# Optimization experiments

Measured on AMD Instinct MI355X. Metric: run time of the kernel, lower is better.

Reference implementation:

```python
import jax, jax.numpy as jnp
import numpy as np

N_NODES = 50000
N_EDGES = 800000
IN_DIM = 128
HID = 256
HEADS = 4
OUT_DIM = 128
NEG_SLOPE = 0.2


def gat_conv(x, src, dst, W, a_src, a_dst, b, heads, out_ch):
    """PyG-style GATConv: per-edge attention + segment softmax over dst."""
    N = x.shape[0]
    h = (x @ W).reshape(N, heads, out_ch)              # [N,H,C]
    alph_s = jnp.einsum('nhc,hc->nh', h, a_src)        # [N,H]
    alph_d = jnp.einsum('nhc,hc->nh', h, a_dst)        # [N,H]
    e = jax.nn.leaky_relu(alph_s[src] + alph_d[dst], NEG_SLOPE)  # [E,H]
    m = jax.lax.stop_gradient(jax.ops.segment_max(e, dst, num_segments=N))
    ex = jnp.exp(e - m[dst])
    s = jax.ops.segment_sum(ex, dst, num_segments=N)
    alpha = ex / (s[dst] + 1e-16)                      # [E,H]
    out = jax.ops.segment_sum(h[src] * alpha[:, :, None], dst, num_segments=N)
    return out.reshape(N, heads * out_ch) + b


def setup_inputs() -> dict:
    key = jax.random.key(0)
    ks = jax.random.split(key, 12)
    x = jax.random.normal(ks[0], (N_NODES, IN_DIM), dtype=jnp.float32)
    edge_index = jax.random.randint(ks[1], (2, N_EDGES), 0, N_NODES, dtype=jnp.int64)
    c1 = HID // HEADS  # 64
    sc1 = 1.0 / np.sqrt(IN_DIM)
    sc2 = 1.0 / np.sqrt(HID)
    W1 = jax.random.normal(ks[2], (IN_DIM, HID), dtype=jnp.float32) * sc1
    a1_src = jax.random.normal(ks[3], (HEADS, c1), dtype=jnp.float32) * sc1
    a1_dst = jax.random.normal(ks[4], (HEADS, c1), dtype=jnp.float32) * sc1
    b1 = jnp.zeros((HID,), dtype=jnp.float32)
    W2 = jax.random.normal(ks[5], (HID, OUT_DIM), dtype=jnp.float32) * sc2
    a2_src = jax.random.normal(ks[6], (1, OUT_DIM), dtype=jnp.float32) * sc2
    a2_dst = jax.random.normal(ks[7], (1, OUT_DIM), dtype=jnp.float32) * sc2
    b2 = jnp.zeros((OUT_DIM,), dtype=jnp.float32)
    return {"x": x, "edge_index": edge_index, "W1": W1, "a1_src": a1_src,
            "a1_dst": a1_dst, "b1": b1, "W2": W2, "a2_src": a2_src,
            "a2_dst": a2_dst, "b2": b2}


def reference(x, edge_index, W1, a1_src, a1_dst, b1, W2, a2_src, a2_dst, b2):
    N = x.shape[0]
    loops = jnp.arange(N, dtype=edge_index.dtype)
    # PyG default add_self_loops=True
    src = jnp.concatenate([edge_index[0], loops])
    dst = jnp.concatenate([edge_index[1], loops])
    h = jax.nn.relu(gat_conv(x, src, dst, W1, a1_src, a1_dst, b1, HEADS, HID // HEADS))
    # dropout is identity in eval mode
    return gat_conv(h, src, dst, W2, a2_src, a2_dst, b2, 1, OUT_DIM)
```

## Files before the change

### kernel.cpp

```cpp
#include <hip/hip_runtime.h>
#include <math.h>

#define NEG_SLOPE 0.2f
#define SLOTS 64

typedef __attribute__((ext_vector_type(8))) short bf16x8;
typedef __attribute__((ext_vector_type(4))) float f32x4;
typedef __attribute__((ext_vector_type(2))) float f32x2;

__device__ __forceinline__ float lrelu(float t) {
    return t > 0.f ? t : NEG_SLOPE * t;
}
__device__ __forceinline__ float bf2f(unsigned short u) {
    return __uint_as_float(((unsigned)u) << 16);
}
__device__ __forceinline__ unsigned short f2bf(float f) {
    unsigned u = __float_as_uint(f);
    unsigned r = (u + 0x7fff + ((u >> 16) & 1)) >> 16;
    return (unsigned short)r;
}
__device__ __forceinline__ int rli(int v, int l) {
    return __builtin_amdgcn_readlane(v, l);
}
__device__ __forceinline__ f32x2 unpack2(unsigned v) {
    f32x2 r;
    r.x = __uint_as_float(v << 16);
    r.y = __uint_as_float(v & 0xffff0000u);
    return r;
}

__global__ void prep(const float* __restrict__ x, unsigned* __restrict__ x_bf2,
                     const float* __restrict__ W1, unsigned short* __restrict__ W1t,
                     const float* __restrict__ W2, unsigned short* __restrict__ W2t,
                     const float* __restrict__ a1s, const float* __restrict__ a1d,
                     float* __restrict__ vsd1,
                     const float* __restrict__ a2s, const float* __restrict__ a2d,
                     float* __restrict__ vsd2,
                     int* __restrict__ cursor, int* __restrict__ eSrc,
                     long nx2, int N, int n0, int n1, int n2, int n3, int n4) {
    const int b = blockIdx.x, t = threadIdx.x;
    if (b < n0) {
        long i = (long)b * 256 + t;
        if (i < nx2) {
            float2 v = ((const float2*)x)[i];
            x_bf2[i] = (unsigned)f2bf(v.x) | ((unsigned)f2bf(v.y) << 16);
        }
    } else if (b < n1) {
        int i = (b - n0) * 256 + t;
        if (i < 256 * 128) {
            int n = i / 128, k = i % 128;
            W1t[i] = f2bf(W1[k * 256 + n]);
        }
    } else if (b < n2) {
        int i = (b - n1) * 256 + t;
        if (i < 128 * 256) {
            int n = i / 256, k = i % 256;
            W2t[i] = f2bf(W2[k * 128 + n]);
        }
    } else if (b < n3) {
        int i = (b - n2) * 256 + t;
        if (i < 512) {
            int k = i / 4, h = i % 4;
            float s = 0.f, d = 0.f;
            for (int c = 0; c < 64; c++) {
                float wv = W1[k * 256 + h * 64 + c];
                s += wv * a1s[h * 64 + c];
                d += wv * a1d[h * 64 + c];
            }
            vsd1[h * 128 + k] = s;
            vsd1[(4 + h) * 128 + k] = d;
        }
    } else if (b < n4) {
        int i = (b - n3) * 256 + t;
        if (i < 256) {
            float s = 0.f, d = 0.f;
            for (int c = 0; c < 128; c++) {
                float wv = W2[i * 128 + c];
                s += wv * a2s[c];
                d += wv * a2d[c];
            }
            vsd2[i] = s;
            vsd2[256 + i] = d;
        }
    } else {
        int i = (b - n4) * 256 + t;
        if (i < N) {
            cursor[i] = 1;
            eSrc[i << 6] = i;
        }
    }
}

__global__ void scatter_edges(const int* __restrict__ src, const int* __restrict__ dst,
                              int* __restrict__ cursor, int* __restrict__ eSrc, int E) {
    int e = blockIdx.x * blockDim.x + threadIdx.x;
    if (e < E) {
        int d = dst[e];
        int pos = atomicAdd(&cursor[d], 1);
        if (pos < SLOTS) eSrc[(d << 6) + pos] = src[e];
    }
}

template <int K, int H>
__global__ void gemv_attn(const float* __restrict__ X, const float* __restrict__ vsd,
                          float* __restrict__ as_, float* __restrict__ ad_, int M) {
    __shared__ float vs[2 * H * K];
    int t = threadIdx.x;
    for (int i = t; i < 2 * H * K; i += 256) vs[i] = vsd[i];
    __syncthreads();
    int wave = t >> 6, lane = t & 63;
    int n = blockIdx.x * 4 + wave;
    if (n >= M) return;
    float acc[2 * H];
#pragma unroll
    for (int j = 0; j < 2 * H; j++) acc[j] = 0.f;
#pragma unroll
    for (int i = 0; i < K / 64; i++) {
        float xv = X[(size_t)n * K + i * 64 + lane];
#pragma unroll
        for (int j = 0; j < 2 * H; j++) acc[j] += xv * vs[j * K + i * 64 + lane];
    }
#pragma unroll
    for (int off = 32; off > 0; off >>= 1) {
#pragma unroll
        for (int j = 0; j < 2 * H; j++) acc[j] += __shfl_down(acc[j], off, 64);
    }
    if (lane == 0) {
#pragma unroll
        for (int h = 0; h < H; h++) {
            as_[n * H + h] = acc[h];
            ad_[n * H + h] = acc[H + h];
        }
    }
}

template <int K, int N>
__global__ __launch_bounds__(256) void gemm_mfma(const unsigned short* __restrict__ A,
                                                 const unsigned short* __restrict__ Bt,
                                                 unsigned short* __restrict__ Cb, int M) {
    constexpr int LDT = 72;
    __shared__ __align__(16) short As[128 * LDT];
    __shared__ __align__(16) short Bs[64 * LDT];
    const int t = threadIdx.x;
    const int wave = t >> 6, lane = t & 63;
    const int row0 = blockIdx.x * 128;
    const int n0 = blockIdx.y * 64;

    f32x4 acc[2][4];
#pragma unroll
    for (int mt = 0; mt < 2; mt++)
#pragma unroll
        for (int nt = 0; nt < 4; nt++) acc[mt][nt] = (f32x4){0.f, 0.f, 0.f, 0.f};

    const int r = t >> 3, c8 = (t & 7) * 8;
    for (int kc = 0; kc < K; kc += 64) {
        const unsigned short* srcA = A + (size_t)row0 * K + kc;
#pragma unroll
        for (int p = 0; p < 4; p++) {
            int rr = r + p * 32;
            *(bf16x8*)&As[rr * LDT + c8] = *(const bf16x8*)&srcA[(size_t)rr * K + c8];
        }
        const unsigned short* srcB = Bt + (size_t)n0 * K + kc;
#pragma unroll
        for (int p = 0; p < 2; p++) {
            int rr = r + p * 32;
            *(bf16x8*)&Bs[rr * LDT + c8] = *(const bf16x8*)&srcB[(size_t)rr * K + c8];
        }
        __syncthreads();

        const int mbase = wave * 32 + (lane & 15);
        const int quad = lane >> 4;
#pragma unroll
        for (int ks = 0; ks < 2; ks++) {
            int ko = ks * 32 + quad * 8;
            bf16x8 a0 = *(const bf16x8*)&As[mbase * LDT + ko];
            bf16x8 a1 = *(const bf16x8*)&As[(mbase + 16) * LDT + ko];
#pragma unroll
            for (int nt = 0; nt < 4; nt++) {
                bf16x8 b = *(const bf16x8*)&Bs[((lane & 15) + nt * 16) * LDT + ko];
                acc[0][nt] = __builtin_amdgcn_mfma_f32_16x16x32_bf16(a0, b, acc[0][nt], 0, 0, 0);
                acc[1][nt] = __builtin_amdgcn_mfma_f32_16x16x32_bf16(a1, b, acc[1][nt], 0, 0, 0);
            }
        }
        __syncthreads();
    }

    const int colb = n0 + (lane & 15);
    const int rquad = (lane >> 4) * 4;
#pragma unroll
    for (int mt = 0; mt < 2; mt++) {
        int rb = row0 + wave * 32 + mt * 16 + rquad;
#pragma unroll
        for (int nt = 0; nt < 4; nt++) {
#pragma unroll
            for (int rr2 = 0; rr2 < 4; rr2++) {
                int row = rb + rr2;
                if (row < M) Cb[(size_t)row * N + colb + nt * 16] = f2bf(acc[mt][nt][rr2]);
            }
        }
    }
}

__global__ __launch_bounds__(256) void gemm1_head(
    const unsigned short* __restrict__ agg, const unsigned short* __restrict__ W1t,
    const float* __restrict__ b1, const float* __restrict__ vsd2,
    unsigned short* __restrict__ out1b, float* __restrict__ as2, float* __restrict__ ad2,
    int M, int Mpad) {
    constexpr int K = 128, LDT = 72;
    __shared__ __align__(16) short As[128 * LDT];
    __shared__ __align__(16) short Bs[64 * LDT];
    const int t = threadIdx.x;
    const int wave = t >> 6, lane = t & 63;
    const int row0 = blockIdx.x * 128;
    const int h = blockIdx.y;
    const unsigned short* A = agg + (size_t)h * Mpad * K;
    const unsigned short* Bt = W1t + (size_t)h * 64 * K;

    f32x4 acc[2][4];
#pragma unroll
    for (int mt = 0; mt < 2; mt++)
#pragma unroll
        for (int nt = 0; nt < 4; nt++) acc[mt][nt] = (f32x4){0.f, 0.f, 0.f, 0.f};

    const int r = t >> 3, c8 = (t & 7) * 8;
    for (int kc = 0; kc < K; kc += 64) {
        const unsigned short* srcA = A + (size_t)row0 * K + kc;
#pragma unroll
        for (int p = 0; p < 4; p++) {
            int rr = r + p * 32;
            *(bf16x8*)&As[rr * LDT + c8] = *(const bf16x8*)&srcA[(size_t)rr * K + c8];
        }
        const unsigned short* srcB = Bt + kc;
#pragma unroll
        for (int p = 0; p < 2; p++) {
            int rr = r + p * 32;
            *(bf16x8*)&Bs[rr * LDT + c8] = *(const bf16x8*)&srcB[(size_t)rr * K + c8];
        }
        __syncthreads();

        const int mbase = wave * 32 + (lane & 15);
        const int quad = lane >> 4;
#pragma unroll
        for (int ks = 0; ks < 2; ks++) {
            int ko = ks * 32 + quad * 8;
            bf16x8 a0 = *(const bf16x8*)&As[mbase * LDT + ko];
            bf16x8 a1 = *(const bf16x8*)&As[(mbase + 16) * LDT + ko];
#pragma unroll
            for (int nt = 0; nt < 4; nt++) {
                bf16x8 b = *(const bf16x8*)&Bs[((lane & 15) + nt * 16) * LDT + ko];
                acc[0][nt] = __builtin_amdgcn_mfma_f32_16x16x32_bf16(a0, b, acc[0][nt], 0, 0, 0);
                acc[1][nt] = __builtin_amdgcn_mfma_f32_16x16x32_bf16(a1, b, acc[1][nt], 0, 0, 0);
            }
        }
        __syncthreads();
    }

    const int col16 = lane & 15;
    const int grp = lane >> 4;
#pragma unroll
    for (int mt = 0; mt < 2; mt++) {
        int rb = row0 + wave * 32 + mt * 16 + grp * 4;
#pragma unroll
        for (int rr = 0; rr < 4; rr++) {
            int row = rb + rr;
            float ps = 0.f, pd = 0.f;
#pragma unroll
            for (int nt = 0; nt < 4; nt++) {
                int cg = h * 64 + col16 + nt * 16;
                float rres = acc[mt][nt][rr] + b1[cg];
                rres = fmaxf(rres, 0.f);
                if (row < M) out1b[(size_t)row * 256 + cg] = f2bf(rres);
                ps += rres * vsd2[cg];
                pd += rres * vsd2[256 + cg];
            }
#pragma unroll
            for (int mask = 1; mask < 16; mask <<= 1) {
                ps += __shfl_xor(ps, mask, 64);
                pd += __shfl_xor(pd, mask, 64);
            }
            if (col16 == 0 && row < M) {
                atomicAdd(&as2[row], ps);
                atomicAdd(&ad2[row], pd);
            }
        }
    }
}

__global__ __launch_bounds__(256) void fused_gather1(
    const int* __restrict__ cursor, const int* __restrict__ eSrc,
    const unsigned short* __restrict__ Xb,
    const float* __restrict__ as_, const float* __restrict__ ad_,
    unsigned short* __restrict__ agg, int N, int Mpad) {
    const int wv = threadIdx.x >> 6, lane = threadIdx.x & 63;
    const int d = blockIdx.x * 4 + wv;
    if (d >= N) return;
    const int beg = d << 6;
    int deg = cursor[d]; deg = deg > SLOTS ? SLOTS : deg;

    __shared__ float4 alS[4][64];

    float4 adv = ((const float4*)ad_)[d];
    const char* Xc = (const char*)Xb;
    const int loff = lane * 4;

    f32x2 acc[4];
#pragma unroll
    for (int h = 0; h < 4; h++) acc[h] = (f32x2){0.f, 0.f};

    bool act = lane < deg;
    int s = act ? eSrc[beg + lane] : 0;
    int esb = s << 8;
    float4 q = act ? ((const float4*)as_)[s] : make_float4(0.f, 0.f, 0.f, 0.f);
    float e0 = act ? lrelu(q.x + adv.x) : -1e30f;
    float e1 = act ? lrelu(q.y + adv.y) : -1e30f;
    float e2 = act ? lrelu(q.z + adv.z) : -1e30f;
    float e3 = act ? lrelu(q.w + adv.w) : -1e30f;
    float m0 = e0, m1 = e1, m2 = e2, m3 = e3;
#pragma unroll
    for (int off = 1; off < 64; off <<= 1) {
        m0 = fmaxf(m0, __shfl_xor(m0, off, 64));
        m1 = fmaxf(m1, __shfl_xor(m1, off, 64));
        m2 = fmaxf(m2, __shfl_xor(m2, off, 64));
        m3 = fmaxf(m3, __shfl_xor(m3, off, 64));
    }
    float x0 = act ? __expf(e0 - m0) : 0.f;
    float x1 = act ? __expf(e1 - m1) : 0.f;
    float x2 = act ? __expf(e2 - m2) : 0.f;
    float x3 = act ? __expf(e3 - m3) : 0.f;
    float s0 = x0, s1 = x1, s2 = x2, s3 = x3;
#pragma unroll
    for (int off = 1; off < 64; off <<= 1) {
        s0 += __shfl_xor(s0, off, 64);
        s1 += __shfl_xor(s1, off, 64);
        s2 += __shfl_xor(s2, off, 64);
        s3 += __shfl_xor(s3, off, 64);
    }
    if (act) {
        float4 av;
        av.x = x0 / (s0 + 1e-16f);
        av.y = x1 / (s1 + 1e-16f);
        av.z = x2 / (s2 + 1e-16f);
        av.w = x3 / (s3 + 1e-16f);
        alS[wv][lane] = av;
    }

    int j = 0;
    for (; j + 3 < deg; j += 4) {
        int o0 = rli(esb, j), o1 = rli(esb, j + 1);
        int o2 = rli(esb, j + 2), o3 = rli(esb, j + 3);
        unsigned v0 = *(const unsigned*)(Xc + o0 + loff);
        unsigned v1 = *(const unsigned*)(Xc + o1 + loff);
        unsigned v2 = *(const unsigned*)(Xc + o2 + loff);
        unsigned v3 = *(const unsigned*)(Xc + o3 + loff);
        float4 al0 = alS[wv][j];
        float4 al1 = alS[wv][j + 1];
        float4 al2 = alS[wv][j + 2];
        float4 al3 = alS[wv][j + 3];
        f32x2 xv0 = unpack2(v0);
        acc[0] += al0.x * xv0; acc[1] += al0.y * xv0;
        acc[2] += al0.z * xv0; acc[3] += al0.w * xv0;
        f32x2 xv1 = unpack2(v1);
        acc[0] += al1.x * xv1; acc[1] += al1.y * xv1;
        acc[2] += al1.z * xv1; acc[3] += al1.w * xv1;
        f32x2 xv2 = unpack2(v2);
        acc[0] += al2.x * xv2; acc[1] += al2.y * xv2;
        acc[2] += al2.z * xv2; acc[3] += al2.w * xv2;
        f32x2 xv3 = unpack2(v3);
        acc[0] += al3.x * xv3; acc[1] += al3.y * xv3;
        acc[2] += al3.z * xv3; acc[3] += al3.w * xv3;
    }
    for (; j < deg; j++) {
        int o0 = rli(esb, j);
        unsigned v0 = *(const unsigned*)(Xc + o0 + loff);
        float4 al0 = alS[wv][j];
        f32x2 xv0 = unpack2(v0);
        acc[0] += al0.x * xv0; acc[1] += al0.y * xv0;
        acc[2] += al0.z * xv0; acc[3] += al0.w * xv0;
    }

#pragma unroll
    for (int h = 0; h < 4; h++) {
        unsigned pack = (unsigned)f2bf(acc[h].x) | ((unsigned)f2bf(acc[h].y) << 16);
        unsigned* p = (unsigned*)(agg + ((size_t)h * Mpad + d) * 128);
        p[lane] = pack;
    }
}

__global__ __launch_bounds__(256) void fused_gather2(
    const int* __restrict__ cursor, const int* __restrict__ eSrc,
    const unsigned short* __restrict__ Hb,
    const float* __restrict__ as_, const float* __restrict__ ad_,
    const float* __restrict__ b2, float* __restrict__ out, int N) {
    const int wv = threadIdx.x >> 6, lane = threadIdx.x & 63;
    const int d = blockIdx.x * 4 + wv;
    if (d >= N) return;
    const int beg = d << 6;
    int deg = cursor[d]; deg = deg > SLOTS ? SLOTS : deg;

    __shared__ float alS[4][64];

    const float adv = ad_[d];
    const char* Hc = (const char*)Hb;
    const int loff = lane * 4;
    f32x2 acc = (f32x2){0.f, 0.f};

    bool act = lane < deg;
    int s = act ? eSrc[beg + lane] : 0;
    int esb = s << 8;
    float e0 = act ? lrelu(as_[s] + adv) : -1e30f;
    float m0 = e0;
#pragma unroll
    for (int off = 1; off < 64; off <<= 1) m0 = fmaxf(m0, __shfl_xor(m0, off, 64));
    float x0 = act ? __expf(e0 - m0) : 0.f;
    float s0 = x0;
#pragma unroll
    for (int off = 1; off < 64; off <<= 1) s0 += __shfl_xor(s0, off, 64);
    if (act) alS[wv][lane] = x0 / (s0 + 1e-16f);

    int j = 0;
    for (; j + 3 < deg; j += 4) {
        int o0 = rli(esb, j), o1 = rli(esb, j + 1);
        int o2 = rli(esb, j + 2), o3 = rli(esb, j + 3);
        unsigned v0 = *(const unsigned*)(Hc + o0 + loff);
        unsigned v1 = *(const unsigned*)(Hc + o1 + loff);
        unsigned v2 = *(const unsigned*)(Hc + o2 + loff);
        unsigned v3 = *(const unsigned*)(Hc + o3 + loff);
        float b0 = alS[wv][j], b1 = alS[wv][j + 1];
        float b2v = alS[wv][j + 2], b3 = alS[wv][j + 3];
        acc += b0 * unpack2(v0);
        acc += b1 * unpack2(v1);
        acc += b2v * unpack2(v2);
        acc += b3 * unpack2(v3);
    }
    for (; j < deg; j++) {
        int o0 = rli(esb, j);
        unsigned v0 = *(const unsigned*)(Hc + o0 + loff);
        acc += alS[wv][j] * unpack2(v0);
    }

    float2 o;
    o.x = acc.x + b2[lane * 2];
    o.y = acc.y + b2[lane * 2 + 1];
    ((float2*)(out + (size_t)d * 128))[lane] = o;
}

extern "C" void kernel_launch(void* const* d_in, const int* in_sizes, int n_in,
                              void* d_out, int out_size, void* d_ws, size_t ws_size,
                              hipStream_t stream) {
    const float* x   = (const float*)d_in[0];
    const int*   ei  = (const int*)d_in[1];
    const float* W1  = (const float*)d_in[2];
    const float* a1s = (const float*)d_in[3];
    const float* a1d = (const float*)d_in[4];
    const float* b1  = (const float*)d_in[5];
    const float* W2  = (const float*)d_in[6];
    const float* a2s = (const float*)d_in[7];
    const float* a2d = (const float*)d_in[8];
    const float* b2  = (const float*)d_in[9];

    const int N = in_sizes[0] / 128;
    const int E = in_sizes[1] / 2;
    const int* srcIdx = ei;
    const int* dstIdx = ei + E;
    float* out = (float*)d_out;

    const int MT = (N + 127) / 128;
    const int M_pad = MT * 128;

    char* w = (char*)d_ws;
    unsigned short* x_bf  = (unsigned short*)w; w += (size_t)N * 128 * 2;
    unsigned short* agg   = (unsigned short*)w; w += (size_t)4 * M_pad * 128 * 2;
    unsigned short* out1b = (unsigned short*)w; w += (size_t)M_pad * 256 * 2;
    unsigned short* h2b   = (unsigned short*)w; w += (size_t)N * 128 * 2;
    unsigned short* W1t   = (unsigned short*)w; w += (size_t)128 * 256 * 2;
    unsigned short* W2t   = (unsigned short*)w; w += (size_t)256 * 128 * 2;
    float* vsd1 = (float*)w; w += (size_t)128 * 8 * 4;
    float* vsd2 = (float*)w; w += (size_t)256 * 2 * 4;
    float* as1  = (float*)w; w += (size_t)N * 4 * 4;
    float* ad1  = (float*)w; w += (size_t)N * 4 * 4;
    float* as2  = (float*)w; w += (size_t)N * 4;
    float* ad2  = (float*)w; w += (size_t)N * 4;
    int* cursor = (int*)w;  w += (size_t)N * 4;
    int* eSrc   = (int*)w;  w += (size_t)N * SLOTS * 4;

    hipMemsetAsync(as2, 0, (size_t)N * 4, stream);
    hipMemsetAsync(ad2, 0, (size_t)N * 4, stream);

    {
        long nx2 = (long)N * 64;
        int c0 = (int)((nx2 + 255) / 256);
        int n0 = c0;
        int n1 = n0 + 128;
        int n2 = n1 + 128;
        int n3 = n2 + 2;
        int n4 = n3 + 1;
        int total = n4 + (N + 255) / 256;
        prep<<<total, 256, 0, stream>>>(x, (unsigned*)x_bf, W1, W1t, W2, W2t,
                                        a1s, a1d, vsd1, a2s, a2d, vsd2,
                                        cursor, eSrc, nx2, N, n0, n1, n2, n3, n4);
    }

    scatter_edges<<<(E + 255) / 256, 256, 0, stream>>>(srcIdx, dstIdx, cursor, eSrc, E);

    gemv_attn<128, 4><<<(N + 3) / 4, 256, 0, stream>>>(x, vsd1, as1, ad1, N);
    fused_gather1<<<(N + 3) / 4, 256, 0, stream>>>(cursor, eSrc, x_bf, as1, ad1, agg, N, M_pad);
    gemm1_head<<<dim3(MT, 4), 256, 0, stream>>>(agg, W1t, b1, vsd2, out1b, as2, ad2, N, M_pad);

    gemm_mfma<256, 128><<<dim3(MT, 2), 256, 0, stream>>>(out1b, W2t, h2b, N);
    fused_gather2<<<(N + 3) / 4, 256, 0, stream>>>(cursor, eSrc, h2b, as2, ad2, b2, out, N);
}
```

Measured before the change: 301.4 us.

## Process two destination nodes per wavefront with 8-byte gathers in GAT aggregation

Both gather kernels now assign one destination node to each 32-lane half of a wavefront instead of a full 64-lane wave. Each lane loads 8 bytes (4 bf16) per neighbor row, and source offsets are staged in LDS instead of read with readlane. The aim is to double useful lanes per wave for average degree around 17, where most of the 64 lanes sat idle, and to widen the memory transactions. In exchange, each half loops to the larger degree of the pair, adding some wasted iterations and extra LDS traffic.

```diff
diff --git a/kernel.cpp b/kernel.cpp
--- a/kernel.cpp
+++ b/kernel.cpp
@@ -10,17 +10,11 @@
 
 __device__ __forceinline__ float lrelu(float t) {
     return t > 0.f ? t : NEG_SLOPE * t;
-}
-__device__ __forceinline__ float bf2f(unsigned short u) {
-    return __uint_as_float(((unsigned)u) << 16);
 }
 __device__ __forceinline__ unsigned short f2bf(float f) {
     unsigned u = __float_as_uint(f);
     unsigned r = (u + 0x7fff + ((u >> 16) & 1)) >> 16;
     return (unsigned short)r;
-}
-__device__ __forceinline__ int rli(int v, int l) {
-    return __builtin_amdgcn_readlane(v, l);
 }
 __device__ __forceinline__ f32x2 unpack2(unsigned v) {
     f32x2 r;
@@ -292,97 +286,131 @@
     const float* __restrict__ as_, const float* __restrict__ ad_,
     unsigned short* __restrict__ agg, int N, int Mpad) {
     const int wv = threadIdx.x >> 6, lane = threadIdx.x & 63;
-    const int d = blockIdx.x * 4 + wv;
-    if (d >= N) return;
+    const int half = lane >> 5, hl = lane & 31;
+    const int d = blockIdx.x * 8 + wv * 2 + half;
+
+    __shared__ float4 alS[4][2][64];
+    __shared__ int offS[4][2][64];
+
+    const bool vn = d < N;
+    int deg = 0;
+    if (vn) { deg = cursor[d]; if (deg > SLOTS) deg = SLOTS; }
+    float4 adv = make_float4(0.f, 0.f, 0.f, 0.f);
+    if (vn) adv = ((const float4*)ad_)[d];
+
     const int beg = d << 6;
-    int deg = cursor[d]; deg = deg > SLOTS ? SLOTS : deg;
-
-    __shared__ float4 alS[4][64];
-
-    float4 adv = ((const float4*)ad_)[d];
+    const int j0 = hl, j1 = hl + 32;
+    const bool a0 = j0 < deg, a1 = j1 < deg;
+    int s0 = vn ? d : 0, s1 = vn ? d : 0;
+    if (a0) s0 = eSrc[beg + j0];
+    if (a1) s1 = eSrc[beg + j1];
+    float4 q0 = make_float4(0.f, 0.f, 0.f, 0.f), q1 = q0;
+    if (a0) q0 = ((const float4*)as_)[s0];
+    if (a1) q1 = ((const float4*)as_)[s1];
+
+    float qa0[4] = {q0.x, q0.y, q0.z, q0.w};
+    float qa1[4] = {q1.x, q1.y, q1.z, q1.w};
+    float ad4[4] = {adv.x, adv.y, adv.z, adv.w};
+    float e0[4], e1[4], m[4];
+#pragma unroll
+    for (int h = 0; h < 4; h++) {
+        e0[h] = a0 ? lrelu(qa0[h] + ad4[h]) : -1e30f;
+        e1[h] = a1 ? lrelu(qa1[h] + ad4[h]) : -1e30f;
+        m[h] = fmaxf(e0[h], e1[h]);
+    }
+#pragma unroll
+    for (int off = 1; off < 32; off <<= 1)
+#pragma unroll
+        for (int h = 0; h < 4; h++) m[h] = fmaxf(m[h], __shfl_xor(m[h], off, 64));
+    float x0[4], x1[4], sum[4];
+#pragma unroll
+    for (int h = 0; h < 4; h++) {
+        x0[h] = a0 ? __expf(e0[h] - m[h]) : 0.f;
+        x1[h] = a1 ? __expf(e1[h] - m[h]) : 0.f;
+        sum[h] = x0[h] + x1[h];
+    }
+#pragma unroll
+    for (int off = 1; off < 32; off <<= 1)
+#pragma unroll
+        for (int h = 0; h < 4; h++) sum[h] += __shfl_xor(sum[h], off, 64);
+    float ri[4];
+#pragma unroll
+    for (int h = 0; h < 4; h++) ri[h] = 1.f / (sum[h] + 1e-16f);
+
+    alS[wv][half][j0] = make_float4(x0[0] * ri[0], x0[1] * ri[1], x0[2] * ri[2], x0[3] * ri[3]);
+    alS[wv][half][j1] = make_float4(x1[0] * ri[0], x1[1] * ri[1], x1[2] * ri[2], x1[3] * ri[3]);
+    offS[wv][half][j0] = s0 << 8;
+    offS[wv][half][j1] = s1 << 8;
+
+    int dmax = deg;
+    { int o = __shfl_xor(dmax, 32, 64); dmax = dmax > o ? dmax : o; }
+
     const char* Xc = (const char*)Xb;
-    const int loff = lane * 4;
-
-    f32x2 acc[4];
-#pragma unroll
-    for (int h = 0; h < 4; h++) acc[h] = (f32x2){0.f, 0.f};
-
-    bool act = lane < deg;
-    int s = act ? eSrc[beg + lane] : 0;
-    int esb = s << 8;
-    float4 q = act ? ((const float4*)as_)[s] : make_float4(0.f, 0.f, 0.f, 0.f);
-    float e0 = act ? lrelu(q.x + adv.x) : -1e30f;
-    float e1 = act ? lrelu(q.y + adv.y) : -1e30f;
-    float e2 = act ? lrelu(q.z + adv.z) : -1e30f;
-    float e3 = act ? lrelu(q.w + adv.w) : -1e30f;
-    float m0 = e0, m1 = e1, m2 = e2, m3 = e3;
-#pragma unroll
-    for (int off = 1; off < 64; off <<= 1) {
-        m0 = fmaxf(m0, __shfl_xor(m0, off, 64));
-        m1 = fmaxf(m1, __shfl_xor(m1, off, 64));
-        m2 = fmaxf(m2, __shfl_xor(m2, off, 64));
-        m3 = fmaxf(m3, __shfl_xor(m3, off, 64));
-    }
-    float x0 = act ? __expf(e0 - m0) : 0.f;
-    float x1 = act ? __expf(e1 - m1) : 0.f;
-    float x2 = act ? __expf(e2 - m2) : 0.f;
-    float x3 = act ? __expf(e3 - m3) : 0.f;
-    float s0 = x0, s1 = x1, s2 = x2, s3 = x3;
-#pragma unroll
-    for (int off = 1; off < 64; off <<= 1) {
-        s0 += __shfl_xor(s0, off, 64);
-        s1 += __shfl_xor(s1, off, 64);
-        s2 += __shfl_xor(s2, off, 64);
-        s3 += __shfl_xor(s3, off, 64);
-    }
-    if (act) {
-        float4 av;
-        av.x = x0 / (s0 + 1e-16f);
-        av.y = x1 / (s1 + 1e-16f);
-        av.z = x2 / (s2 + 1e-16f);
-        av.w = x3 / (s3 + 1e-16f);
-        alS[wv][lane] = av;
-    }
+    const int myoff = hl * 8;
+    f32x2 acc[4][2];
+#pragma unroll
+    for (int h = 0; h < 4; h++) { acc[h][0] = (f32x2){0.f, 0.f}; acc[h][1] = (f32x2){0.f, 0.f}; }
 
     int j = 0;
-    for (; j + 3 < deg; j += 4) {
-        int o0 = rli(esb, j), o1 = rli(esb, j + 1);
-        int o2 = rli(esb, j + 2), o3 = rli(esb, j + 3);
-        unsigned v0 = *(const unsigned*)(Xc + o0 + loff);
-        unsigned v1 = *(const unsigned*)(Xc + o1 + loff);
-        unsigned v2 = *(const unsigned*)(Xc + o2 + loff);
-        unsigned v3 = *(const unsigned*)(Xc + o3 + loff);
-        float4 al0 = alS[wv][j];
-        float4 al1 = alS[wv][j + 1];
-        float4 al2 = alS[wv][j + 2];
-        float4 al3 = alS[wv][j + 3];
-        f32x2 xv0 = unpack2(v0);
-        acc[0] += al0.x * xv0; acc[1] += al0.y * xv0;
-        acc[2] += al0.z * xv0; acc[3] += al0.w * xv0;
-        f32x2 xv1 = unpack2(v1);
-        acc[0] += al1.x * xv1; acc[1] += al1.y * xv1;
-        acc[2] += al1.z * xv1; acc[3] += al1.w * xv1;
-        f32x2 xv2 = unpack2(v2);
-        acc[0] += al2.x * xv2; acc[1] += al2.y * xv2;
-        acc[2] += al2.z * xv2; acc[3] += al2.w * xv2;
-        f32x2 xv3 = unpack2(v3);
-        acc[0] += al3.x * xv3; acc[1] += al3.y * xv3;
-        acc[2] += al3.z * xv3; acc[3] += al3.w * xv3;
-    }
-    for (; j < deg; j++) {
-        int o0 = rli(esb, j);
-        unsigned v0 = *(const unsigned*)(Xc + o0 + loff);
-        float4 al0 = alS[wv][j];
-        f32x2 xv0 = unpack2(v0);
-        acc[0] += al0.x * xv0; acc[1] += al0.y * xv0;
-        acc[2] += al0.z * xv0; acc[3] += al0.w * xv0;
-    }
-
-#pragma unroll
-    for (int h = 0; h < 4; h++) {
-        unsigned pack = (unsigned)f2bf(acc[h].x) | ((unsigned)f2bf(acc[h].y) << 16);
-        unsigned* p = (unsigned*)(agg + ((size_t)h * Mpad + d) * 128);
-        p[lane] = pack;
+    for (; j + 3 < dmax; j += 4) {
+        int o0 = offS[wv][half][j], o1 = offS[wv][half][j + 1];
+        int o2 = offS[wv][half][j + 2], o3 = offS[wv][half][j + 3];
+        uint2 v0 = *(const uint2*)(Xc + o0 + myoff);
+        uint2 v1 = *(const uint2*)(Xc + o1 + myoff);
+        uint2 v2 = *(const uint2*)(Xc + o2 + myoff);
+        uint2 v3 = *(const uint2*)(Xc + o3 + myoff);
+        float4 al0 = alS[wv][half][j];
+        float4 al1 = alS[wv][half][j + 1];
+        float4 al2 = alS[wv][half][j + 2];
+        float4 al3 = alS[wv][half][j + 3];
+        {
+            f32x2 lo = unpack2(v0.x), hi = unpack2(v0.y);
+            acc[0][0] += al0.x * lo; acc[0][1] += al0.x * hi;
+            acc[1][0] += al0.y * lo; acc[1][1] += al0.y * hi;
+            acc[2][0] += al0.z * lo; acc[2][1] += al0.z * hi;
+            acc[3][0] += al0.w * lo; acc[3][1] += al0.w * hi;
+        }
+        {
+            f32x2 lo = unpack2(v1.x), hi = unpack2(v1.y);
+            acc[0][0] += al1.x * lo; acc[0][1] += al1.x * hi;
+            acc[1][0] += al1.y * lo; acc[1][1] += al1.y * hi;
+            acc[2][0] += al1.z * lo; acc[2][1] += al1.z * hi;
+            acc[3][0] += al1.w * lo; acc[3][1] += al1.w * hi;
+        }
+        {
+            f32x2 lo = unpack2(v2.x), hi = unpack2(v2.y);
+            acc[0][0] += al2.x * lo; acc[0][1] += al2.x * hi;
+            acc[1][0] += al2.y * lo; acc[1][1] += al2.y * hi;
+            acc[2][0] += al2.z * lo; acc[2][1] += al2.z * hi;
+            acc[3][0] += al2.w * lo; acc[3][1] += al2.w * hi;
+        }
+        {
+            f32x2 lo = unpack2(v3.x), hi = unpack2(v3.y);
+            acc[0][0] += al3.x * lo; acc[0][1] += al3.x * hi;
+            acc[1][0] += al3.y * lo; acc[1][1] += al3.y * hi;
+            acc[2][0] += al3.z * lo; acc[2][1] += al3.z * hi;
+            acc[3][0] += al3.w * lo; acc[3][1] += al3.w * hi;
+        }
+    }
+    for (; j < dmax; j++) {
+        int o0 = offS[wv][half][j];
+        uint2 v0 = *(const uint2*)(Xc + o0 + myoff);
+        float4 al0 = alS[wv][half][j];
+        f32x2 lo = unpack2(v0.x), hi = unpack2(v0.y);
+        acc[0][0] += al0.x * lo; acc[0][1] += al0.x * hi;
+        acc[1][0] += al0.y * lo; acc[1][1] += al0.y * hi;
+        acc[2][0] += al0.z * lo; acc[2][1] += al0.z * hi;
+        acc[3][0] += al0.w * lo; acc[3][1] += al0.w * hi;
+    }
+
+    if (vn) {
+#pragma unroll
+        for (int h = 0; h < 4; h++) {
+            uint2 pack;
+            pack.x = (unsigned)f2bf(acc[h][0].x) | ((unsigned)f2bf(acc[h][0].y) << 16);
+            pack.y = (unsigned)f2bf(acc[h][1].x) | ((unsigned)f2bf(acc[h][1].y) << 16);
+            ((uint2*)(agg + ((size_t)h * Mpad + d) * 128))[hl] = pack;
+        }
     }
 }
 
@@ -392,56 +420,78 @@
     const float* __restrict__ as_, const float* __restrict__ ad_,
     const float* __restrict__ b2, float* __restrict__ out, int N) {
     const int wv = threadIdx.x >> 6, lane = threadIdx.x & 63;
-    const int d = blockIdx.x * 4 + wv;
-    if (d >= N) return;
+    const int half = lane >> 5, hl = lane & 31;
+    const int d = blockIdx.x * 8 + wv * 2 + half;
+
+    __shared__ float alS[4][2][64];
+    __shared__ int offS[4][2][64];
+
+    const bool vn = d < N;
+    int deg = 0;
+    if (vn) { deg = cursor[d]; if (deg > SLOTS) deg = SLOTS; }
+    const float adv = vn ? ad_[d] : 0.f;
+
     const int beg = d << 6;
-    int deg = cursor[d]; deg = deg > SLOTS ? SLOTS : deg;
-
-    __shared__ float alS[4][64];
-
-    const float adv = ad_[d];
+    const int j0 = hl, j1 = hl + 32;
+    const bool a0 = j0 < deg, a1 = j1 < deg;
+    int s0 = vn ? d : 0, s1 = vn ? d : 0;
+    if (a0) s0 = eSrc[beg + j0];
+    if (a1) s1 = eSrc[beg + j1];
+    float e0 = a0 ? lrelu(as_[s0] + adv) : -1e30f;
+    float e1 = a1 ? lrelu(as_[s1] + adv) : -1e30f;
+    float m = fmaxf(e0, e1);
+#pragma unroll
+    for (int off = 1; off < 32; off <<= 1) m = fmaxf(m, __shfl_xor(m, off, 64));
+    float x0 = a0 ? __expf(e0 - m) : 0.f;
+    float x1 = a1 ? __expf(e1 - m) : 0.f;
+    float sum = x0 + x1;
+#pragma unroll
+    for (int off = 1; off < 32; off <<= 1) sum += __shfl_xor(sum, off, 64);
+    float ri = 1.f / (sum + 1e-16f);
+
+    alS[wv][half][j0] = x0 * ri;
+    alS[wv][half][j1] = x1 * ri;
+    offS[wv][half][j0] = s0 << 8;
+    offS[wv][half][j1] = s1 << 8;
+
+    int dmax = deg;
+    { int o = __shfl_xor(dmax, 32, 64); dmax = dmax > o ? dmax : o; }
+
     const char* Hc = (const char*)Hb;
-    const int loff = lane * 4;
-    f32x2 acc = (f32x2){0.f, 0.f};
-
-    bool act = lane < deg;
-    int s = act ? eSrc[beg + lane] : 0;
-    int esb = s << 8;
-    float e0 = act ? lrelu(as_[s] + adv) : -1e30f;
-    float m0 = e0;
-#pragma unroll
-    for (int off = 1; off < 64; off <<= 1) m0 = fmaxf(m0, __shfl_xor(m0, off, 64));
-    float x0 = act ? __expf(e0 - m0) : 0.f;
-    float s0 = x0;
-#pragma unroll
-    for (int off = 1; off < 64; off <<= 1) s0 += __shfl_xor(s0, off, 64);
-    if (act) alS[wv][lane] = x0 / (s0 + 1e-16f);
+    const int myoff = hl * 8;
+    f32x2 acc0 = (f32x2){0.f, 0.f}, acc1 = (f32x2){0.f, 0.f};
 
     int j = 0;
-    for (; j + 3 < deg; j += 4) {
-        int o0 = rli(esb, j), o1 = rli(esb, j + 1);
-        int o2 = rli(esb, j + 2), o3 = rli(esb, j + 3);
-        unsigned v0 = *(const unsigned*)(Hc + o0 + loff);
-        unsigned v1 = *(const unsigned*)(Hc + o1 + loff);
-        unsigned v2 = *(const unsigned*)(Hc + o2 + loff);
-        unsigned v3 = *(const unsigned*)(Hc + o3 + loff);
-        float b0 = alS[wv][j], b1 = alS[wv][j + 1];
-        float b2v = alS[wv][j + 2], b3 = alS[wv][j + 3];
-        acc += b0 * unpack2(v0);
-        acc += b1 * unpack2(v1);
-        acc += b2v * unpack2(v2);
-        acc += b3 * unpack2(v3);
-    }
-    for (; j < deg; j++) {
-        int o0 = rli(esb, j);
-        unsigned v0 = *(const unsigned*)(Hc + o0 + loff);
-        acc += alS[wv][j] * unpack2(v0);
-    }
-
-    float2 o;
-    o.x = acc.x + b2[lane * 2];
-    o.y = acc.y + b2[lane * 2 + 1];
-    ((float2*)(out + (size_t)d * 128))[lane] = o;
+    for (; j + 3 < dmax; j += 4) {
+        int o0 = offS[wv][half][j], o1 = offS[wv][half][j + 1];
+        int o2 = offS[wv][half][j + 2], o3 = offS[wv][half][j + 3];
+        uint2 v0 = *(const uint2*)(Hc + o0 + myoff);
+        uint2 v1 = *(const uint2*)(Hc + o1 + myoff);
+        uint2 v2 = *(const uint2*)(Hc + o2 + myoff);
+        uint2 v3 = *(const uint2*)(Hc + o3 + myoff);
+        float b0 = alS[wv][half][j], b1v = alS[wv][half][j + 1];
+        float b2v = alS[wv][half][j + 2], b3 = alS[wv][half][j + 3];
+        acc0 += b0 * unpack2(v0.x); acc1 += b0 * unpack2(v0.y);
+        acc0 += b1v * unpack2(v1.x); acc1 += b1v * unpack2(v1.y);
+        acc0 += b2v * unpack2(v2.x); acc1 += b2v * unpack2(v2.y);
+        acc0 += b3 * unpack2(v3.x); acc1 += b3 * unpack2(v3.y);
+    }
+    for (; j < dmax; j++) {
+        int o0 = offS[wv][half][j];
+        uint2 v0 = *(const uint2*)(Hc + o0 + myoff);
+        float b0 = alS[wv][half][j];
+        acc0 += b0 * unpack2(v0.x); acc1 += b0 * unpack2(v0.y);
+    }
+
+    if (vn) {
+        float4 bb = ((const float4*)b2)[hl];
+        float4 o;
+        o.x = acc0.x + bb.x;
+        o.y = acc0.y + bb.y;
+        o.z = acc1.x + bb.z;
+        o.w = acc1.y + bb.w;
+        ((float4*)(out + (size_t)d * 128))[hl] = o;
+    }
 }
 
 extern "C" void kernel_launch(void* const* d_in, const int* in_sizes, int n_in,
@@ -503,9 +553,9 @@
     scatter_edges<<<(E + 255) / 256, 256, 0, stream>>>(srcIdx, dstIdx, cursor, eSrc, E);
 
     gemv_attn<128, 4><<<(N + 3) / 4, 256, 0, stream>>>(x, vsd1, as1, ad1, N);
-    fused_gather1<<<(N + 3) / 4, 256, 0, stream>>>(cursor, eSrc, x_bf, as1, ad1, agg, N, M_pad);
+    fused_gather1<<<(N + 7) / 8, 256, 0, stream>>>(cursor, eSrc, x_bf, as1, ad1, agg, N, M_pad);
     gemm1_head<<<dim3(MT, 4), 256, 0, stream>>>(agg, W1t, b1, vsd2, out1b, as2, ad2, N, M_pad);
 
     gemm_mfma<256, 128><<<dim3(MT, 2), 256, 0, stream>>>(out1b, W2t, h2b, N);
-    fused_gather2<<<(N + 3) / 4, 256, 0, stream>>>(cursor, eSrc, h2b, as2, ad2, b2, out, N);
-}
+    fused_gather2<<<(N + 7) / 8, 256, 0, stream>>>(cursor, eSrc, h2b, as2, ad2, b2, out, N);
+}
```

Measured after the change: 292.8 us. 1.03x faster.
